# Kernel optimization log

Measured on AMD Instinct MI355X. Metric: run time of the kernel, lower is better.

Reference implementation:

```python
import jax, jax.numpy as jnp
import numpy as np

D_MODEL = 1024
NUM_HEADS = 16
DEPTH = D_MODEL // NUM_HEADS
B, S = 4, 2048


def setup_inputs() -> dict:
    key = jax.random.key(0)
    ks = jax.random.split(key, 12)
    s = 1.0 / np.sqrt(D_MODEL)
    return {
        "q": jax.random.normal(ks[0], (B, S, D_MODEL), jnp.float32),
        "k": jax.random.normal(ks[1], (B, S, D_MODEL), jnp.float32),
        "v": jax.random.normal(ks[2], (B, S, D_MODEL), jnp.float32),
        "mask": jax.random.randint(ks[3], (B, S), 0, 2, jnp.int32),
        "wq_w": jax.random.uniform(ks[4], (D_MODEL, D_MODEL), jnp.float32, -s, s),
        "wq_b": jnp.zeros((D_MODEL,), jnp.float32),
        "wk_w": jax.random.uniform(ks[5], (D_MODEL, D_MODEL), jnp.float32, -s, s),
        "wk_b": jnp.zeros((D_MODEL,), jnp.float32),
        "wv_w": jax.random.uniform(ks[6], (D_MODEL, D_MODEL), jnp.float32, -s, s),
        "wv_b": jnp.zeros((D_MODEL,), jnp.float32),
        "wo_w": jax.random.uniform(ks[7], (D_MODEL, D_MODEL), jnp.float32, -s, s),
        "wo_b": jnp.zeros((D_MODEL,), jnp.float32),
    }


def _split_heads(x):
    # [B, S, D] -> [B, H, S, depth]
    b, s, _ = x.shape
    return x.reshape(b, s, NUM_HEADS, DEPTH).transpose(0, 2, 1, 3)


def reference(q, k, v, mask, wq_w, wq_b, wk_w, wk_b, wv_w, wv_b, wo_w, wo_b):
    qh = _split_heads(q @ wq_w.T + wq_b)
    kh = _split_heads(k @ wk_w.T + wk_b)
    vh = _split_heads(v @ wv_w.T + wv_b)
    # [B, H, Sq, Sk]
    logits = jnp.einsum("bhqd,bhkd->bhqk", qh, kh) / jnp.sqrt(
        jnp.asarray(DEPTH, jnp.float32))
    # 2D mask -> [B, 1, 1, Sk], masked_fill where mask == 0
    m = mask[:, None, None, :]
    logits = jnp.where(m == 0, jnp.asarray(-1e9, logits.dtype), logits)
    attn = jax.nn.softmax(logits, axis=-1)
    out = jnp.einsum("bhqk,bhkd->bhqd", attn, vh)
    out = out.transpose(0, 2, 1, 3).reshape(q.shape[0], -1, D_MODEL)
    return out @ wo_w.T + wo_b
```

## Files before the change

kernel.cpp:

```cpp
#include <hip/hip_runtime.h>
#include <hip/hip_bf16.h>
#include <stdint.h>

typedef __bf16 bf16_t;
typedef __bf16 bf16x8 __attribute__((ext_vector_type(8)));
typedef __bf16 bf16x2 __attribute__((ext_vector_type(2)));
typedef float  f32x4  __attribute__((ext_vector_type(4)));
typedef float  f32x16 __attribute__((ext_vector_type(16)));
typedef unsigned int u32;
typedef u32 u32x4 __attribute__((ext_vector_type(4)));

#define D_MODEL 1024
#define NHEAD   16
#define DEPTH   64
#define BATCH   4
#define SEQ     2048
#define MROWS   (BATCH*SEQ)

#define SC 0.18033688011112042f

__device__ __forceinline__ void gload16(const void* g, void* l) {
    __builtin_amdgcn_global_load_lds(
        (__attribute__((address_space(1))) void*)(uintptr_t)g,
        (__attribute__((address_space(3))) void*)l,
        16, 0, 0);
}

__device__ __forceinline__ u32 pk2(float a, float b) {
    bf16x2 t; t[0] = (bf16_t)a; t[1] = (bf16_t)b;
    return __builtin_bit_cast(u32, t);
}

__global__ __launch_bounds__(256) void cvt3_kernel(const float* __restrict__ s0, bf16_t* __restrict__ d0,
                                                   const float* __restrict__ s1, bf16_t* __restrict__ d1,
                                                   const float* __restrict__ s2, bf16_t* __restrict__ d2,
                                                   int n8) {
    int i = blockIdx.x * 256 + threadIdx.x;
    if (i >= n8) return;
    const float* src; bf16_t* dst;
    switch (blockIdx.y) {
        case 0: src = s0; dst = d0; break;
        case 1: src = s1; dst = d1; break;
        default: src = s2; dst = d2; break;
    }
    const float4* s4 = (const float4*)src;
    float4 a = s4[2*(size_t)i], b = s4[2*(size_t)i + 1];
    bf16x8 o;
    o[0] = (bf16_t)a.x; o[1] = (bf16_t)a.y; o[2] = (bf16_t)a.z; o[3] = (bf16_t)a.w;
    o[4] = (bf16_t)b.x; o[5] = (bf16_t)b.y; o[6] = (bf16_t)b.z; o[7] = (bf16_t)b.w;
    *(bf16x8*)(dst + 8*(size_t)i) = o;
}

__global__ __launch_bounds__(256) void cvtw_kernel(const float* __restrict__ s0, bf16_t* __restrict__ d0,
                                                   const float* __restrict__ s1, bf16_t* __restrict__ d1,
                                                   const float* __restrict__ s2, bf16_t* __restrict__ d2,
                                                   const float* __restrict__ s3, bf16_t* __restrict__ d3,
                                                   int n8) {
    int i = blockIdx.x * 256 + threadIdx.x;
    if (i >= n8) return;
    const float* src; bf16_t* dst;
    switch (blockIdx.y) {
        case 0: src = s0; dst = d0; break;
        case 1: src = s1; dst = d1; break;
        case 2: src = s2; dst = d2; break;
        default: src = s3; dst = d3; break;
    }
    const float4* s4 = (const float4*)src;
    float4 a = s4[2*(size_t)i], b = s4[2*(size_t)i + 1];
    bf16x8 o;
    o[0] = (bf16_t)a.x; o[1] = (bf16_t)a.y; o[2] = (bf16_t)a.z; o[3] = (bf16_t)a.w;
    o[4] = (bf16_t)b.x; o[5] = (bf16_t)b.y; o[6] = (bf16_t)b.z; o[7] = (bf16_t)b.w;
    *(bf16x8*)(dst + 8*(size_t)i) = o;
}

template<int MODE>
__global__ __launch_bounds__(256) void gemm_bt(const bf16_t* __restrict__ A,
                                               const bf16_t* __restrict__ Bw,
                                               const float* __restrict__ bias,
                                               bf16_t* __restrict__ Cb,
                                               float* __restrict__ Cf,
                                               int M, int N, int K, float scale) {
    __shared__ bf16_t Smem[2*128*64];
    bf16_t* As = Smem;
    bf16_t* Bs = Smem + 128*64;
    const int tid  = threadIdx.x;
    const int wave = tid >> 6, lane = tid & 63;
    const int lr = lane & 15, lk = (lane >> 4) * 8;
    const int bm = (blockIdx.x >> 3) * 128, bn = (blockIdx.x & 7) * 128;
    const int wr = (wave >> 1) * 64, wc = (wave & 1) * 64;

    f32x4 acc[4][4] = {};

    for (int kt = 0; kt < K; kt += 64) {
#pragma unroll
        for (int p = 0; p < 4; ++p) {
            int chunk = p*256 + tid;
            int r  = chunk >> 3;
            int cs = ((chunk & 7) ^ (r & 7)) * 8;
            gload16(A  + (size_t)(bm + r)*K + kt + cs, As + (size_t)(p*256 + wave*64)*8);
            gload16(Bw + (size_t)(bn + r)*K + kt + cs, Bs + (size_t)(p*256 + wave*64)*8);
        }
        __syncthreads();
        const char* AsB = (const char*)As;
        const char* BsB = (const char*)Bs;
#pragma unroll
        for (int ks = 0; ks < 2; ++ks) {
            int kb = (ks*32 + lk) * 2;
            bf16x8 af[4], bfv[4];
#pragma unroll
            for (int mi = 0; mi < 4; ++mi) {
                int row = wr + mi*16 + lr;
                af[mi] = *(const bf16x8*)(AsB + ((row*128 + kb) ^ ((row & 7) << 4)));
            }
#pragma unroll
            for (int ni = 0; ni < 4; ++ni) {
                int row = wc + ni*16 + lr;
                bfv[ni] = *(const bf16x8*)(BsB + ((row*128 + kb) ^ ((row & 7) << 4)));
            }
            __builtin_amdgcn_s_setprio(1);
#pragma unroll
            for (int mi = 0; mi < 4; ++mi)
#pragma unroll
                for (int ni = 0; ni < 4; ++ni)
                    acc[mi][ni] = __builtin_amdgcn_mfma_f32_16x16x32_bf16(
                        af[mi], bfv[ni], acc[mi][ni], 0, 0, 0);
            __builtin_amdgcn_s_setprio(0);
        }
        __syncthreads();
    }

    if (MODE != 2) {
#pragma unroll
        for (int ni = 0; ni < 4; ++ni) {
            int col = bn + wc + ni*16 + lr;
            float bv = bias[col];
#pragma unroll
            for (int mi = 0; mi < 4; ++mi) {
#pragma unroll
                for (int j = 0; j < 4; ++j) {
                    int row = bm + wr + mi*16 + (lane >> 4)*4 + j;
                    float vv = (acc[mi][ni][j] + bv) * scale;
                    if (MODE == 1) Cb[(size_t)row*N + col] = (bf16_t)vv;
                    else           Cf[(size_t)row*N + col] = vv;
                }
            }
        }
    } else {
        char* TB = (char*)Smem;
#pragma unroll
        for (int ni = 0; ni < 4; ++ni) {
            int col = wc + ni*16 + lr;
            int swz = (col & 7) << 4;
            float bv = bias[bn + col];
#pragma unroll
            for (int mi = 0; mi < 4; ++mi)
#pragma unroll
                for (int j = 0; j < 4; ++j) {
                    int row = wr + mi*16 + (lane >> 4)*4 + j;
                    int sp  = (row & ~12) | ((row & 4) << 1) | ((row & 8) >> 1);
                    float vv = (acc[mi][ni][j] + bv) * scale;
                    *(bf16_t*)(TB + ((col*256 + sp*2) ^ swz)) = (bf16_t)vv;
                }
        }
        __syncthreads();
        const int b = bm >> 11, sl = bm & 2047;
#pragma unroll
        for (int p = 0; p < 8; ++p) {
            int id = p*256 + tid;
            int col = id >> 4, sg = id & 15;
            bf16x8 v8 = *(const bf16x8*)(TB + ((col*256 + sg*16) ^ ((col & 7) << 4)));
            int gc = bn + col;
            int bh = b*16 + (gc >> 6), d = gc & 63;
            *(bf16x8*)&Cb[((size_t)bh*DEPTH + d)*SEQ + sl + sg*8] = v8;
        }
    }
}

__global__ __launch_bounds__(256, 3) void attn_kernel(const bf16_t* __restrict__ Qp,
                                                      const bf16_t* __restrict__ Kp,
                                                      const bf16_t* __restrict__ Vt,
                                                      const int* __restrict__ mask,
                                                      bf16_t* __restrict__ AO) {
    __shared__ bf16_t Ks[3][64*64];
    __shared__ bf16_t Vs[3][64*64];
    __shared__ bf16_t mbias[SEQ];

    const int tid  = threadIdx.x;
    const int wave = tid >> 6, lane = tid & 63;
    const int lr5 = lane & 31;
    const int hi  = lane >> 5;

    const int flat = blockIdx.x + 16*blockIdx.y + 256*blockIdx.z;
    const int xcd = flat & 7, slot = flat >> 3;
    const int bh = xcd + 8*(slot >> 4);
    const int b = bh >> 4, h = bh & 15;
    const int q0 = (slot & 15) * 128;

    const int qw = q0 + wave*32;
    const size_t base  = (size_t)b * SEQ * D_MODEL + (size_t)h * DEPTH;
    const size_t vbase = (size_t)bh * DEPTH * SEQ;

    bf16x8 qf[4];
#pragma unroll
    for (int dc = 0; dc < 4; ++dc)
        qf[dc] = *(const bf16x8*)&Qp[base + (size_t)(qw + lr5)*D_MODEL + dc*16 + hi*8];

    u32x4 onew = {};
    onew[0] = hi ? 0u : 0x3F80u;
    const bf16x8 qone = __builtin_bit_cast(bf16x8, onew);

    {
        const int4* mp = (const int4*)&mask[(size_t)b*SEQ + tid*8];
        int4 m0 = mp[0], m1 = mp[1];
        bf16x8 mm;
        mm[0] = (m0.x == 0) ? (bf16_t)(-1e30f) : (bf16_t)0.0f;
        mm[1] = (m0.y == 0) ? (bf16_t)(-1e30f) : (bf16_t)0.0f;
        mm[2] = (m0.z == 0) ? (bf16_t)(-1e30f) : (bf16_t)0.0f;
        mm[3] = (m0.w == 0) ? (bf16_t)(-1e30f) : (bf16_t)0.0f;
        mm[4] = (m1.x == 0) ? (bf16_t)(-1e30f) : (bf16_t)0.0f;
        mm[5] = (m1.y == 0) ? (bf16_t)(-1e30f) : (bf16_t)0.0f;
        mm[6] = (m1.z == 0) ? (bf16_t)(-1e30f) : (bf16_t)0.0f;
        mm[7] = (m1.w == 0) ? (bf16_t)(-1e30f) : (bf16_t)0.0f;
        *(bf16x8*)&mbias[tid*8] = mm;
    }

    auto stage = [&](int t, int buf) {
#pragma unroll
        for (int p = 0; p < 2; ++p) {
            int chunk = p*256 + tid; int r = chunk >> 3;
            int cs = ((chunk & 7) ^ (r & 7)) * 8;
            gload16(Kp + base + (size_t)(t*64 + r)*D_MODEL + cs,
                    (bf16_t*)Ks[buf] + (size_t)chunk*8);
            gload16(Vt + vbase + (size_t)r*SEQ + t*64 + cs,
                    (bf16_t*)Vs[buf] + (size_t)chunk*8);
        }
    };

    f32x16 o0 = {}, o1 = {};
    float l_run = 0.f;

    stage(0, 0); stage(1, 1); stage(2, 2);
    asm volatile("s_waitcnt vmcnt(8) lgkmcnt(0)");
    __builtin_amdgcn_s_barrier();

    int cb = 0;
    for (int t = 0; t < SEQ/64; ++t) {
        u32 mw0 = (u32)__builtin_bit_cast(unsigned short, mbias[t*64 + lr5]);
        u32 mw1 = (u32)__builtin_bit_cast(unsigned short, mbias[t*64 + 32 + lr5]);
        if (hi) { mw0 = 0; mw1 = 0; }
        u32x4 mv0 = {}, mv1 = {};
        mv0[0] = mw0; mv1[0] = mw1;
        bf16x8 afm0 = __builtin_bit_cast(bf16x8, mv0);
        bf16x8 afm1 = __builtin_bit_cast(bf16x8, mv1);

        const char* KsB = (const char*)Ks[cb];
        const f32x16 zz = {};
        f32x16 s0, s1;
        __builtin_amdgcn_s_setprio(1);
        s0 = __builtin_amdgcn_mfma_f32_32x32x16_bf16(afm0, qone, zz, 0, 0, 0);
        s1 = __builtin_amdgcn_mfma_f32_32x32x16_bf16(afm1, qone, zz, 0, 0, 0);
#pragma unroll
        for (int dc = 0; dc < 4; ++dc) {
            int colb = dc*32 + hi*16;
            int row0 = lr5, row1 = 32 + lr5;
            bf16x8 kf0 = *(const bf16x8*)(KsB + ((row0*128 + colb) ^ ((row0 & 7) << 4)));
            bf16x8 kf1 = *(const bf16x8*)(KsB + ((row1*128 + colb) ^ ((row1 & 7) << 4)));
            s0 = __builtin_amdgcn_mfma_f32_32x32x16_bf16(kf0, qf[dc], s0, 0, 0, 0);
            s1 = __builtin_amdgcn_mfma_f32_32x32x16_bf16(kf1, qf[dc], s1, 0, 0, 0);
        }
        __builtin_amdgcn_s_setprio(0);

        const char* VsB = (const char*)Vs[cb];
#pragma unroll
        for (int kt = 0; kt < 2; ++kt) {
            const f32x16& sh = kt ? s1 : s0;
            float pv[16];
#pragma unroll
            for (int r = 0; r < 16; ++r) pv[r] = __builtin_exp2f(sh[r]);
            float su0 = 0.f, su1 = 0.f, su2 = 0.f, su3 = 0.f;
#pragma unroll
            for (int r = 0; r < 16; r += 4) {
                su0 += pv[r]; su1 += pv[r+1]; su2 += pv[r+2]; su3 += pv[r+3];
            }
            l_run += (su0 + su1) + (su2 + su3);
#pragma unroll
            for (int c = 0; c < 2; ++c) {
                u32x4 fwv;
#pragma unroll
                for (int i = 0; i < 4; ++i)
                    fwv[i] = pk2(pv[c*8 + 2*i], pv[c*8 + 2*i + 1]);
                bf16x8 pfrag = __builtin_bit_cast(bf16x8, fwv);
                int colb = kt*64 + c*32 + hi*16;
                int row0 = lr5, row1 = 32 + lr5;
                bf16x8 vf0 = *(const bf16x8*)(VsB + ((row0*128 + colb) ^ ((row0 & 7) << 4)));
                bf16x8 vf1 = *(const bf16x8*)(VsB + ((row1*128 + colb) ^ ((row1 & 7) << 4)));
                __builtin_amdgcn_s_setprio(1);
                o0 = __builtin_amdgcn_mfma_f32_32x32x16_bf16(vf0, pfrag, o0, 0, 0, 0);
                o1 = __builtin_amdgcn_mfma_f32_32x32x16_bf16(vf1, pfrag, o1, 0, 0, 0);
                __builtin_amdgcn_s_setprio(0);
            }
        }

        asm volatile("s_waitcnt vmcnt(4) lgkmcnt(0)");
        __builtin_amdgcn_s_barrier();
        if (t + 3 < SEQ/64) stage(t + 3, cb);
        ++cb; if (cb == 3) cb = 0;
    }

    float l_tot = l_run + __shfl_xor(l_run, 32);
    float inv = 1.f / l_tot;
    char* TrB = (char*)Ks;
    const int qloc = wave*32 + lr5;
#pragma unroll
    for (int mt = 0; mt < 2; ++mt)
#pragma unroll
        for (int r = 0; r < 16; ++r) {
            int d = mt*32 + (r & 3) + 8*(r >> 2) + 4*hi;
            float val = (mt ? o1[r] : o0[r]) * inv;
            *(bf16_t*)(TrB + (qloc*128 + ((d*2) ^ ((qloc & 7) << 4)))) = (bf16_t)val;
        }
    __syncthreads();
#pragma unroll
    for (int p = 0; p < 4; ++p) {
        int id = p*256 + tid;
        int row = id >> 3, g = id & 7;
        bf16x8 v8 = *(const bf16x8*)(TrB + (row*128 + ((g*16) ^ ((row & 7) << 4))));
        *(bf16x8*)&AO[base + (size_t)(q0 + row)*D_MODEL + g*8] = v8;
    }
}

extern "C" void kernel_launch(void* const* d_in, const int* in_sizes, int n_in,
                              void* d_out, int out_size, void* d_ws, size_t ws_size,
                              hipStream_t stream) {
    (void)in_sizes; (void)n_in; (void)out_size; (void)ws_size;
    const float* q    = (const float*)d_in[0];
    const float* k    = (const float*)d_in[1];
    const float* v    = (const float*)d_in[2];
    const int*   mask = (const int*)d_in[3];
    const float* wq_w = (const float*)d_in[4];
    const float* wq_b = (const float*)d_in[5];
    const float* wk_w = (const float*)d_in[6];
    const float* wk_b = (const float*)d_in[7];
    const float* wv_w = (const float*)d_in[8];
    const float* wv_b = (const float*)d_in[9];
    const float* wo_w = (const float*)d_in[10];
    const float* wo_b = (const float*)d_in[11];
    float* out = (float*)d_out;

    const size_t ACT = (size_t)MROWS * D_MODEL;
    const size_t WSZ = (size_t)D_MODEL * D_MODEL;
    bf16_t* B0 = (bf16_t*)d_ws;
    bf16_t* B1 = B0 + ACT;
    bf16_t* B2 = B1 + ACT;
    bf16_t* B3 = B2 + ACT;
    bf16_t* Wq = B3 + ACT;
    bf16_t* Wk = Wq + WSZ;
    bf16_t* Wv = Wk + WSZ;
    bf16_t* Wo = Wv + WSZ;

    const int wn8 = (int)(WSZ/8), an8 = (int)(ACT/8);
    cvtw_kernel<<<dim3(wn8/256, 4), dim3(256), 0, stream>>>(wq_w, Wq, wk_w, Wk, wv_w, Wv, wo_w, Wo, wn8);
    cvt3_kernel<<<dim3(an8/256, 3), dim3(256), 0, stream>>>(q, B0, k, B1, v, B2, an8);

    const int ggrid = (MROWS/128) * (D_MODEL/128);
    gemm_bt<1><<<ggrid, dim3(256), 0, stream>>>(B0, Wq, wq_b, B3, nullptr, MROWS, D_MODEL, D_MODEL, SC);
    gemm_bt<1><<<ggrid, dim3(256), 0, stream>>>(B1, Wk, wk_b, B0, nullptr, MROWS, D_MODEL, D_MODEL, 1.f);
    gemm_bt<2><<<ggrid, dim3(256), 0, stream>>>(B2, Wv, wv_b, B1, nullptr, MROWS, D_MODEL, D_MODEL, 1.f);

    attn_kernel<<<dim3(SEQ/128, NHEAD, BATCH), dim3(256), 0, stream>>>(B3, B0, B1, mask, B2);

    gemm_bt<0><<<ggrid, dim3(256), 0, stream>>>(B2, Wo, wo_b, nullptr, out, MROWS, D_MODEL, D_MODEL, 1.f);
}
```

Before: 231.2 us.

## Process two query sub-tiles per attention block to reuse staged K/V

Each attention block now handles 256 query rows (two 128-row sub-tiles) instead of 128, so every K/V tile staged into LDS feeds twice as many MFMAs, and the grid shrinks by half. The goal is to halve K/V global traffic and staging overhead per unit of work. The cost is more registers per thread for the extra accumulators and Q fragments, possible occupancy loss under launch_bounds(256,3), and only 512 blocks to spread across CUs. The GEMM LDS destination index is also simplified to chunk*8, which computes the same address.

```diff
diff --git a/kernel.cpp b/kernel.cpp
--- a/kernel.cpp
+++ b/kernel.cpp
@@ -97,8 +97,8 @@
             int chunk = p*256 + tid;
             int r  = chunk >> 3;
             int cs = ((chunk & 7) ^ (r & 7)) * 8;
-            gload16(A  + (size_t)(bm + r)*K + kt + cs, As + (size_t)(p*256 + wave*64)*8);
-            gload16(Bw + (size_t)(bn + r)*K + kt + cs, Bs + (size_t)(p*256 + wave*64)*8);
+            gload16(A  + (size_t)(bm + r)*K + kt + cs, As + (size_t)chunk*8);
+            gload16(Bw + (size_t)(bn + r)*K + kt + cs, Bs + (size_t)chunk*8);
         }
         __syncthreads();
         const char* AsB = (const char*)As;
@@ -190,20 +190,22 @@
     const int lr5 = lane & 31;
     const int hi  = lane >> 5;
 
-    const int flat = blockIdx.x + 16*blockIdx.y + 256*blockIdx.z;
+    const int flat = blockIdx.x + 8*blockIdx.y + 128*blockIdx.z;
     const int xcd = flat & 7, slot = flat >> 3;
-    const int bh = xcd + 8*(slot >> 4);
+    const int bh = xcd + 8*(slot >> 3);
     const int b = bh >> 4, h = bh & 15;
-    const int q0 = (slot & 15) * 128;
-
-    const int qw = q0 + wave*32;
+    const int q0 = (slot & 7) * 256;
+
     const size_t base  = (size_t)b * SEQ * D_MODEL + (size_t)h * DEPTH;
     const size_t vbase = (size_t)bh * DEPTH * SEQ;
 
-    bf16x8 qf[4];
-#pragma unroll
-    for (int dc = 0; dc < 4; ++dc)
-        qf[dc] = *(const bf16x8*)&Qp[base + (size_t)(qw + lr5)*D_MODEL + dc*16 + hi*8];
+    bf16x8 qf[2][4];
+#pragma unroll
+    for (int qs = 0; qs < 2; ++qs)
+#pragma unroll
+        for (int dc = 0; dc < 4; ++dc)
+            qf[qs][dc] = *(const bf16x8*)&Qp[base +
+                (size_t)(q0 + qs*128 + wave*32 + lr5)*D_MODEL + dc*16 + hi*8];
 
     u32x4 onew = {};
     onew[0] = hi ? 0u : 0x3F80u;
@@ -236,8 +238,9 @@
         }
     };
 
-    f32x16 o0 = {}, o1 = {};
-    float l_run = 0.f;
+    f32x16 oA0 = {}, oA1 = {};
+    f32x16 oB0 = {}, oB1 = {};
+    float lA = 0.f, lB = 0.f;
 
     stage(0, 0); stage(1, 1); stage(2, 2);
     asm volatile("s_waitcnt vmcnt(8) lgkmcnt(0)");
@@ -254,51 +257,62 @@
         bf16x8 afm1 = __builtin_bit_cast(bf16x8, mv1);
 
         const char* KsB = (const char*)Ks[cb];
-        const f32x16 zz = {};
-        f32x16 s0, s1;
-        __builtin_amdgcn_s_setprio(1);
-        s0 = __builtin_amdgcn_mfma_f32_32x32x16_bf16(afm0, qone, zz, 0, 0, 0);
-        s1 = __builtin_amdgcn_mfma_f32_32x32x16_bf16(afm1, qone, zz, 0, 0, 0);
-#pragma unroll
-        for (int dc = 0; dc < 4; ++dc) {
-            int colb = dc*32 + hi*16;
-            int row0 = lr5, row1 = 32 + lr5;
-            bf16x8 kf0 = *(const bf16x8*)(KsB + ((row0*128 + colb) ^ ((row0 & 7) << 4)));
-            bf16x8 kf1 = *(const bf16x8*)(KsB + ((row1*128 + colb) ^ ((row1 & 7) << 4)));
-            s0 = __builtin_amdgcn_mfma_f32_32x32x16_bf16(kf0, qf[dc], s0, 0, 0, 0);
-            s1 = __builtin_amdgcn_mfma_f32_32x32x16_bf16(kf1, qf[dc], s1, 0, 0, 0);
-        }
-        __builtin_amdgcn_s_setprio(0);
-
         const char* VsB = (const char*)Vs[cb];
-#pragma unroll
-        for (int kt = 0; kt < 2; ++kt) {
-            const f32x16& sh = kt ? s1 : s0;
-            float pv[16];
-#pragma unroll
-            for (int r = 0; r < 16; ++r) pv[r] = __builtin_exp2f(sh[r]);
-            float su0 = 0.f, su1 = 0.f, su2 = 0.f, su3 = 0.f;
-#pragma unroll
-            for (int r = 0; r < 16; r += 4) {
-                su0 += pv[r]; su1 += pv[r+1]; su2 += pv[r+2]; su3 += pv[r+3];
-            }
-            l_run += (su0 + su1) + (su2 + su3);
-#pragma unroll
-            for (int c = 0; c < 2; ++c) {
-                u32x4 fwv;
-#pragma unroll
-                for (int i = 0; i < 4; ++i)
-                    fwv[i] = pk2(pv[c*8 + 2*i], pv[c*8 + 2*i + 1]);
-                bf16x8 pfrag = __builtin_bit_cast(bf16x8, fwv);
-                int colb = kt*64 + c*32 + hi*16;
+
+#pragma unroll
+        for (int qs = 0; qs < 2; ++qs) {
+            const f32x16 zz = {};
+            f32x16 s0, s1;
+            __builtin_amdgcn_s_setprio(1);
+            s0 = __builtin_amdgcn_mfma_f32_32x32x16_bf16(afm0, qone, zz, 0, 0, 0);
+            s1 = __builtin_amdgcn_mfma_f32_32x32x16_bf16(afm1, qone, zz, 0, 0, 0);
+#pragma unroll
+            for (int dc = 0; dc < 4; ++dc) {
+                int colb = dc*32 + hi*16;
                 int row0 = lr5, row1 = 32 + lr5;
-                bf16x8 vf0 = *(const bf16x8*)(VsB + ((row0*128 + colb) ^ ((row0 & 7) << 4)));
-                bf16x8 vf1 = *(const bf16x8*)(VsB + ((row1*128 + colb) ^ ((row1 & 7) << 4)));
-                __builtin_amdgcn_s_setprio(1);
-                o0 = __builtin_amdgcn_mfma_f32_32x32x16_bf16(vf0, pfrag, o0, 0, 0, 0);
-                o1 = __builtin_amdgcn_mfma_f32_32x32x16_bf16(vf1, pfrag, o1, 0, 0, 0);
-                __builtin_amdgcn_s_setprio(0);
-            }
+                bf16x8 kf0 = *(const bf16x8*)(KsB + ((row0*128 + colb) ^ ((row0 & 7) << 4)));
+                bf16x8 kf1 = *(const bf16x8*)(KsB + ((row1*128 + colb) ^ ((row1 & 7) << 4)));
+                s0 = __builtin_amdgcn_mfma_f32_32x32x16_bf16(kf0, qf[qs][dc], s0, 0, 0, 0);
+                s1 = __builtin_amdgcn_mfma_f32_32x32x16_bf16(kf1, qf[qs][dc], s1, 0, 0, 0);
+            }
+            __builtin_amdgcn_s_setprio(0);
+
+            float lsum = 0.f;
+#pragma unroll
+            for (int kt = 0; kt < 2; ++kt) {
+                const f32x16& sh = kt ? s1 : s0;
+                float pv[16];
+#pragma unroll
+                for (int r = 0; r < 16; ++r) pv[r] = __builtin_exp2f(sh[r]);
+                float su0 = 0.f, su1 = 0.f, su2 = 0.f, su3 = 0.f;
+#pragma unroll
+                for (int r = 0; r < 16; r += 4) {
+                    su0 += pv[r]; su1 += pv[r+1]; su2 += pv[r+2]; su3 += pv[r+3];
+                }
+                lsum += (su0 + su1) + (su2 + su3);
+#pragma unroll
+                for (int c = 0; c < 2; ++c) {
+                    u32x4 fwv;
+#pragma unroll
+                    for (int i = 0; i < 4; ++i)
+                        fwv[i] = pk2(pv[c*8 + 2*i], pv[c*8 + 2*i + 1]);
+                    bf16x8 pfrag = __builtin_bit_cast(bf16x8, fwv);
+                    int colb = kt*64 + c*32 + hi*16;
+                    int row0 = lr5, row1 = 32 + lr5;
+                    bf16x8 vf0 = *(const bf16x8*)(VsB + ((row0*128 + colb) ^ ((row0 & 7) << 4)));
+                    bf16x8 vf1 = *(const bf16x8*)(VsB + ((row1*128 + colb) ^ ((row1 & 7) << 4)));
+                    __builtin_amdgcn_s_setprio(1);
+                    if (qs == 0) {
+                        oA0 = __builtin_amdgcn_mfma_f32_32x32x16_bf16(vf0, pfrag, oA0, 0, 0, 0);
+                        oA1 = __builtin_amdgcn_mfma_f32_32x32x16_bf16(vf1, pfrag, oA1, 0, 0, 0);
+                    } else {
+                        oB0 = __builtin_amdgcn_mfma_f32_32x32x16_bf16(vf0, pfrag, oB0, 0, 0, 0);
+                        oB1 = __builtin_amdgcn_mfma_f32_32x32x16_bf16(vf1, pfrag, oB1, 0, 0, 0);
+                    }
+                    __builtin_amdgcn_s_setprio(0);
+                }
+            }
+            if (qs == 0) lA += lsum; else lB += lsum;
         }
 
         asm volatile("s_waitcnt vmcnt(4) lgkmcnt(0)");
@@ -307,25 +321,31 @@
         ++cb; if (cb == 3) cb = 0;
     }
 
-    float l_tot = l_run + __shfl_xor(l_run, 32);
-    float inv = 1.f / l_tot;
     char* TrB = (char*)Ks;
     const int qloc = wave*32 + lr5;
 #pragma unroll
-    for (int mt = 0; mt < 2; ++mt)
-#pragma unroll
-        for (int r = 0; r < 16; ++r) {
-            int d = mt*32 + (r & 3) + 8*(r >> 2) + 4*hi;
-            float val = (mt ? o1[r] : o0[r]) * inv;
-            *(bf16_t*)(TrB + (qloc*128 + ((d*2) ^ ((qloc & 7) << 4)))) = (bf16_t)val;
-        }
-    __syncthreads();
-#pragma unroll
-    for (int p = 0; p < 4; ++p) {
-        int id = p*256 + tid;
-        int row = id >> 3, g = id & 7;
-        bf16x8 v8 = *(const bf16x8*)(TrB + (row*128 + ((g*16) ^ ((row & 7) << 4))));
-        *(bf16x8*)&AO[base + (size_t)(q0 + row)*D_MODEL + g*8] = v8;
+    for (int qs = 0; qs < 2; ++qs) {
+        if (qs) __syncthreads();
+        float lr_ = (qs == 0) ? lA : lB;
+        float l_tot = lr_ + __shfl_xor(lr_, 32);
+        float inv = 1.f / l_tot;
+#pragma unroll
+        for (int mt = 0; mt < 2; ++mt)
+#pragma unroll
+            for (int r = 0; r < 16; ++r) {
+                int d = mt*32 + (r & 3) + 8*(r >> 2) + 4*hi;
+                float val = (qs == 0 ? (mt ? oA1[r] : oA0[r])
+                                     : (mt ? oB1[r] : oB0[r])) * inv;
+                *(bf16_t*)(TrB + (qloc*128 + ((d*2) ^ ((qloc & 7) << 4)))) = (bf16_t)val;
+            }
+        __syncthreads();
+#pragma unroll
+        for (int p = 0; p < 4; ++p) {
+            int id = p*256 + tid;
+            int row = id >> 3, g = id & 7;
+            bf16x8 v8 = *(const bf16x8*)(TrB + (row*128 + ((g*16) ^ ((row & 7) << 4))));
+            *(bf16x8*)&AO[base + (size_t)(q0 + qs*128 + row)*D_MODEL + g*8] = v8;
+        }
     }
 }
 
@@ -367,7 +387,7 @@
     gemm_bt<1><<<ggrid, dim3(256), 0, stream>>>(B1, Wk, wk_b, B0, nullptr, MROWS, D_MODEL, D_MODEL, 1.f);
     gemm_bt<2><<<ggrid, dim3(256), 0, stream>>>(B2, Wv, wv_b, B1, nullptr, MROWS, D_MODEL, D_MODEL, 1.f);
 
-    attn_kernel<<<dim3(SEQ/128, NHEAD, BATCH), dim3(256), 0, stream>>>(B3, B0, B1, mask, B2);
+    attn_kernel<<<dim3(SEQ/256, NHEAD, BATCH), dim3(256), 0, stream>>>(B3, B0, B1, mask, B2);
 
     gemm_bt<0><<<ggrid, dim3(256), 0, stream>>>(B2, Wo, wo_b, nullptr, out, MROWS, D_MODEL, D_MODEL, 1.f);
 }
```

Result: slower. 386.7 us (+67.2%).
